# Optimization experiments

Measured on AMD Instinct MI355X. Metric: run time of the kernel, lower is better.

Reference implementation:

```python
import jax, jax.numpy as jnp
import numpy as np

B, A, F, T = 4096, 64, 124, 8
H1, H2 = 64, 16


def setup_inputs() -> dict:
    key = jax.random.key(0)
    ks = jax.random.split(key, 10)
    x = jax.random.normal(ks[0], (B, A, F + 1), dtype=jnp.float32)
    types = jax.random.randint(ks[1], (B, A), 0, T).astype(jnp.float32)
    x = x.at[:, :, 0].set(types)  # column 0 stores atom-type index
    mask = (jax.random.uniform(ks[2], (B, A)) < 0.9).astype(jnp.float32)
    s1 = 1.0 / np.sqrt(F)
    s2 = 1.0 / np.sqrt(H1)
    s3 = 1.0 / np.sqrt(H2)
    return {
        "x_padded": x,
        "mask": mask,
        "W1": jax.random.normal(ks[3], (T, F, H1), dtype=jnp.float32) * s1,
        "b1": jax.random.normal(ks[4], (T, H1), dtype=jnp.float32) * s1,
        "W2": jax.random.normal(ks[5], (T, H1, H2), dtype=jnp.float32) * s2,
        "b2": jax.random.normal(ks[6], (T, H2), dtype=jnp.float32) * s2,
        "W3": jax.random.normal(ks[7], (T, H2, 1), dtype=jnp.float32) * s3,
        "b3": jax.random.normal(ks[8], (T, 1), dtype=jnp.float32) * s3,
    }


def reference(x_padded, mask, W1, b1, W2, b2, W3, b3):
    # x_padded: [B, A, 1+F]; mask: [B, A]
    type_idx = x_padded[:, :, 0].astype(jnp.int32)           # [B, A]
    feats = x_padded[:, :, 1:]                               # [B, A, F]
    n_types = W1.shape[0]
    # Faithful to the original: every type's subnet runs on the FULL batch
    # with non-matching atoms zero-masked (bias paths still contribute).
    type_mask = (type_idx[None, :, :] == jnp.arange(n_types)[:, None, None]).astype(feats.dtype)  # [T,B,A]
    sel = feats[None, :, :, :] * type_mask[..., None]        # [T,B,A,F]
    h = jax.nn.relu(jnp.einsum('tbaf,tfh->tbah', sel, W1) + b1[:, None, None, :])
    h = jax.nn.relu(jnp.einsum('tbah,thg->tbag', h, W2) + b2[:, None, None, :])
    o = jnp.einsum('tbag,tgo->tbao', h, W3) + b3[:, None, None, :]  # [T,B,A,1]
    per_atom = (o[..., 0] * mask[None, :, :]).sum(axis=0)   # [B, A]
    return per_atom.sum(axis=1, keepdims=True)               # [B, 1]
```

## Files before the change

### kernel.cpp

```cpp
#include <hip/hip_runtime.h>
#include <stdint.h>

#define NMOL 4096
#define NATOMS (NMOL * 64)
#define NF 124
#define NT 8
#define ROWV 125
#define CAP 65536

#define WS_DCONST  0
#define WS_CURSOR  64
#define WS_W1S     128
#define WS_W2T     131200
#define WS_LIST    147712

#define HS 72

typedef __attribute__((ext_vector_type(8))) short short8;
typedef __attribute__((ext_vector_type(4))) float floatx4;
typedef __attribute__((ext_vector_type(4), aligned(4))) float floatx4u;
typedef __attribute__((ext_vector_type(4))) unsigned int uint4v;

__device__ __forceinline__ unsigned short f2bf(float f) {
    unsigned u = __builtin_bit_cast(unsigned, f);
    u += 0x7fffu + ((u >> 16) & 1u);
    return (unsigned short)(u >> 16);
}
__device__ __forceinline__ unsigned pk2(float a, float b) {
    return (unsigned)f2bf(a) | ((unsigned)f2bf(b) << 16);
}
__device__ __forceinline__ void ld_lds16(const void* g, void* lds) {
    __builtin_amdgcn_global_load_lds(
        (const __attribute__((address_space(1))) unsigned int*)g,
        (__attribute__((address_space(3))) unsigned int*)lds, 16, 0, 0);
}

__global__ __launch_bounds__(256) void k_setup(const float* __restrict__ W1,
                                               const float* __restrict__ b1,
                                               const float* __restrict__ W2,
                                               const float* __restrict__ b2,
                                               const float* __restrict__ W3,
                                               const float* __restrict__ b3,
                                               float* __restrict__ dconst,
                                               unsigned* __restrict__ cursor,
                                               unsigned short* __restrict__ W1S,
                                               unsigned short* __restrict__ W2T,
                                               float* __restrict__ out) {
    int tid = threadIdx.x, b = blockIdx.x;
    if (b == 0) {
        __shared__ float c[NT];
        if (tid < 128) {
            int t = tid >> 4, g = tid & 15;
            float acc = b2[t * 16 + g];
            for (int h = 0; h < 64; ++h) {
                float h1 = b1[t * 64 + h];
                h1 = h1 > 0.f ? h1 : 0.f;
                acc += h1 * W2[(size_t)t * 1024 + h * 16 + g];
            }
            float h2 = acc > 0.f ? acc : 0.f;
            float v = h2 * W3[t * 16 + g];
            #pragma unroll
            for (int off = 1; off < 16; off <<= 1) v += __shfl_xor(v, off);
            if (g == 0) c[t] = v + b3[t];
        }
        if (tid < NT) cursor[tid] = (unsigned)(tid * CAP);
        __syncthreads();
        if (tid == 0) {
            float T_ = 0.f;
            for (int i = 0; i < NT; ++i) T_ += c[i];
            for (int i = 0; i < NT; ++i) dconst[i] = T_ - c[i] + b3[i];
        }
    } else if (b <= 8) {
        int t = b - 1;
        const float* w1g = W1 + (size_t)t * NF * 64;
        unsigned short* dst = W1S + (size_t)t * 8192;
        for (int id = tid; id < 1024; id += 256) {
            int h = id >> 4, cc = id & 15;
            unsigned u[4];
            #pragma unroll
            for (int j = 0; j < 4; ++j) {
                int f0 = cc * 8 + 2 * j;
                unsigned short lo = (f0 < NF)     ? f2bf(w1g[f0 * 64 + h])       : (unsigned short)0;
                unsigned short hi = (f0 + 1 < NF) ? f2bf(w1g[(f0 + 1) * 64 + h]) : (unsigned short)0;
                u[j] = (unsigned)lo | ((unsigned)hi << 16);
            }
            int p = cc ^ (h & 15);
            *(uint4v*)(dst + h * 128 + p * 8) = (uint4v){u[0], u[1], u[2], u[3]};
        }
        unsigned short* d2 = W2T + (size_t)t * 1024;
        for (int i = tid; i < 1024; i += 256) {
            int g = i >> 6, h = i & 63;
            d2[i] = f2bf(W2[(size_t)t * 1024 + h * 16 + g]);
        }
    } else {
        out[(b - 9) * 256 + tid] = 0.0f;
    }
}

__global__ __launch_bounds__(256) void k_sort(const float* __restrict__ x,
                                              const float* __restrict__ mask,
                                              unsigned* __restrict__ cursor,
                                              unsigned* __restrict__ list) {
    __shared__ unsigned hist[NT], basep[NT], cur[NT];
    int tid = threadIdx.x;
    if (tid < NT) { hist[tid] = 0u; cur[tid] = 0u; }
    __syncthreads();
    int base = blockIdx.x * 1024;
    unsigned char tb[4];
    for (int i = 0; i < 4; ++i) {
        int atom = base + i * 256 + tid;
        float tf = x[(size_t)atom * ROWV];
        float m  = mask[atom];
        tb[i] = 0xFF;
        if (m != 0.0f) { tb[i] = (unsigned char)(int)tf; atomicAdd(&hist[tb[i]], 1u); }
    }
    __syncthreads();
    if (tid < NT && hist[tid]) basep[tid] = atomicAdd(&cursor[tid], hist[tid]);
    __syncthreads();
    for (int i = 0; i < 4; ++i) {
        if (tb[i] != 0xFF) {
            unsigned p = basep[tb[i]] + atomicAdd(&cur[tb[i]], 1u);
            list[p] = (unsigned)(base + i * 256 + tid);
        }
    }
}

__global__ __launch_bounds__(256, 4) void k_mlp(const float* __restrict__ x,
                                                const unsigned short* __restrict__ W1S,
                                                const float* __restrict__ b1,
                                                const unsigned short* __restrict__ W2T,
                                                const float* __restrict__ b2,
                                                const float* __restrict__ W3,
                                                const unsigned* __restrict__ cursor,
                                                const float* __restrict__ dconst,
                                                const unsigned* __restrict__ list,
                                                float* __restrict__ out) {
    __shared__ unsigned short sW[64 * 128];
    __shared__ unsigned short sH[128 * HS];
    __shared__ unsigned sIds[128];

    int t    = blockIdx.x >> 9;
    int tile = blockIdx.x & 511;
    int cnt  = (int)(cursor[t] - (unsigned)(t * CAP));
    int valid = cnt - (tile << 7);
    if (valid <= 0) return;
    if (valid > 128) valid = 128;
    int rowstart = t * CAP + (tile << 7);

    int tid  = threadIdx.x;
    int wv   = tid >> 6;
    int lane = tid & 63;
    int quad = lane >> 4, l15 = lane & 15;
    int rowbase = wv * 32;

    {
        const char* src = (const char*)W1S + (size_t)t * 16384 + wv * 4096 + lane * 16;
        char*       dst = (char*)sW + wv * 4096;
        #pragma unroll
        for (int i = 0; i < 4; ++i) ld_lds16(src + i * 1024, dst + i * 1024);
    }
    if (tid < 128) sIds[tid] = list[rowstart + (tid < valid ? tid : 0)];

    float b1v[4];
    #pragma unroll
    for (int n = 0; n < 4; ++n) b1v[n] = b1[t * 64 + n * 16 + l15];

    __syncthreads();

    short8 afrag[2][4];
    #pragma unroll
    for (int m = 0; m < 2; ++m) {
        unsigned atom = sIds[rowbase + m * 16 + l15];
        const float* rp = x + (size_t)atom * ROWV + 1;
        #pragma unroll
        for (int ks = 0; ks < 4; ++ks) {
            int k0 = ks * 32 + quad * 8;
            floatx4 f0 = (floatx4)(*(const floatx4u*)(rp + k0));
            floatx4 f1 = (floatx4)0.f;
            if (!(ks == 3 && quad == 3))
                f1 = (floatx4)(*(const floatx4u*)(rp + k0 + 4));
            uint4v uu = (uint4v){pk2(f0[0], f0[1]), pk2(f0[2], f0[3]),
                                 pk2(f1[0], f1[1]), pk2(f1[2], f1[3])};
            afrag[m][ks] = __builtin_bit_cast(short8, uu);
        }
    }

    floatx4 c1[2][4];
    #pragma unroll
    for (int m = 0; m < 2; ++m)
        #pragma unroll
        for (int n = 0; n < 4; ++n) c1[m][n] = (floatx4)0.f;

    #pragma unroll
    for (int ks = 0; ks < 4; ++ks) {
        short8 bf[4];
        #pragma unroll
        for (int n = 0; n < 4; ++n)
            bf[n] = *(const short8*)(sW + (n * 16 + l15) * 128 + (((ks * 4 + quad) ^ l15) << 3));
        #pragma unroll
        for (int n = 0; n < 4; ++n) {
            c1[0][n] = __builtin_amdgcn_mfma_f32_16x16x32_bf16(afrag[0][ks], bf[n], c1[0][n], 0, 0, 0);
            c1[1][n] = __builtin_amdgcn_mfma_f32_16x16x32_bf16(afrag[1][ks], bf[n], c1[1][n], 0, 0, 0);
        }
    }

    #pragma unroll
    for (int m = 0; m < 2; ++m)
        #pragma unroll
        for (int n = 0; n < 4; ++n) {
            int col = n * 16 + l15;
            #pragma unroll
            for (int r = 0; r < 4; ++r) {
                float v = c1[m][n][r] + b1v[n];
                v = v > 0.f ? v : 0.f;
                sH[(rowbase + m * 16 + quad * 4 + r) * HS + col] = f2bf(v);
            }
        }

    const unsigned short* w2t = W2T + (size_t)t * 1024;
    floatx4 c2[2];
    c2[0] = (floatx4)0.f; c2[1] = (floatx4)0.f;
    #pragma unroll
    for (int ks = 0; ks < 2; ++ks) {
        int ko = ks * 32 + quad * 8;
        short8 a0 = *(const short8*)(sH + (rowbase + l15) * HS + ko);
        short8 a1 = *(const short8*)(sH + (rowbase + 16 + l15) * HS + ko);
        short8 bw = *(const short8*)(w2t + l15 * 64 + ko);
        c2[0] = __builtin_amdgcn_mfma_f32_16x16x32_bf16(a0, bw, c2[0], 0, 0, 0);
        c2[1] = __builtin_amdgcn_mfma_f32_16x16x32_bf16(a1, bw, c2[1], 0, 0, 0);
    }

    float b2v = b2[t * 16 + l15];
    float w3v = W3[t * 16 + l15];
    float dct = dconst[t];
    #pragma unroll
    for (int m = 0; m < 2; ++m) {
        float h2v[4];
        #pragma unroll
        for (int r = 0; r < 4; ++r) {
            float v = c2[m][r] + b2v;
            v = v > 0.f ? v : 0.f;
            h2v[r] = v * w3v;
        }
        #pragma unroll
        for (int off = 1; off < 16; off <<= 1)
            #pragma unroll
            for (int r = 0; r < 4; ++r) h2v[r] += __shfl_xor(h2v[r], off);
        if (l15 == 0) {
            #pragma unroll
            for (int r = 0; r < 4; ++r) {
                int row = rowbase + m * 16 + quad * 4 + r;
                if (row < valid) {
                    unsigned atom = sIds[row];
                    atomicAdd(&out[atom >> 6], h2v[r] + dct);
                }
            }
        }
    }
}

extern "C" void kernel_launch(void* const* d_in, const int* in_sizes, int n_in,
                              void* d_out, int out_size, void* d_ws, size_t ws_size,
                              hipStream_t stream) {
    const float* x    = (const float*)d_in[0];
    const float* mask = (const float*)d_in[1];
    const float* W1   = (const float*)d_in[2];
    const float* b1   = (const float*)d_in[3];
    const float* W2   = (const float*)d_in[4];
    const float* b2   = (const float*)d_in[5];
    const float* W3   = (const float*)d_in[6];
    const float* b3   = (const float*)d_in[7];
    float* out = (float*)d_out;

    char* ws = (char*)d_ws;
    float*          dconst = (float*)(ws + WS_DCONST);
    unsigned*       cursor = (unsigned*)(ws + WS_CURSOR);
    unsigned short* W1S    = (unsigned short*)(ws + WS_W1S);
    unsigned short* W2T    = (unsigned short*)(ws + WS_W2T);
    unsigned*       list   = (unsigned*)(ws + WS_LIST);

    k_setup<<<25, 256, 0, stream>>>(W1, b1, W2, b2, W3, b3, dconst, cursor, W1S, W2T, out);
    k_sort<<<256, 256, 0, stream>>>(x, mask, cursor, list);
    k_mlp<<<NT * (CAP / 128), 256, 0, stream>>>(x, W1S, b1, W2T, b2, W3,
                                                cursor, dconst, list, out);
}
```

Measured before the change: 217.3 us.

## Load W1 MFMA fragments directly from global, drop LDS staging and block barrier

Pre-packs W1 in setup into a fragment-ordered layout so each lane can read its MFMA B operand straight from global/L2 instead of staging the 16KB weight tile into LDS. Atom ids move from an LDS array into registers and are distributed with wave shuffles, which removes the block-wide barrier. The lower LDS footprint lets the launch bound rise from 4 to 6 blocks per SIMD for more occupancy. The cost is repeated global or cache reads of the weights by every wave, and possible register pressure under the tighter bound.

Result: slower. 234.3 us (+7.9%).

```diff
diff --git a/kernel.cpp b/kernel.cpp
--- a/kernel.cpp
+++ b/kernel.cpp
@@ -10,7 +10,7 @@
 
 #define WS_DCONST  0
 #define WS_CURSOR  64
-#define WS_W1S     128
+#define WS_W1G     128
 #define WS_W2T     131200
 #define WS_LIST    147712
 
@@ -28,11 +28,6 @@
 }
 __device__ __forceinline__ unsigned pk2(float a, float b) {
     return (unsigned)f2bf(a) | ((unsigned)f2bf(b) << 16);
-}
-__device__ __forceinline__ void ld_lds16(const void* g, void* lds) {
-    __builtin_amdgcn_global_load_lds(
-        (const __attribute__((address_space(1))) unsigned int*)g,
-        (__attribute__((address_space(3))) unsigned int*)lds, 16, 0, 0);
 }
 
 __global__ __launch_bounds__(256) void k_setup(const float* __restrict__ W1,
@@ -43,7 +38,7 @@
                                                const float* __restrict__ b3,
                                                float* __restrict__ dconst,
                                                unsigned* __restrict__ cursor,
-                                               unsigned short* __restrict__ W1S,
+                                               unsigned short* __restrict__ W1G,
                                                unsigned short* __restrict__ W2T,
                                                float* __restrict__ out) {
     int tid = threadIdx.x, b = blockIdx.x;
@@ -73,19 +68,20 @@
     } else if (b <= 8) {
         int t = b - 1;
         const float* w1g = W1 + (size_t)t * NF * 64;
-        unsigned short* dst = W1S + (size_t)t * 8192;
+        unsigned short* dst = W1G + (size_t)t * 8192;
         for (int id = tid; id < 1024; id += 256) {
-            int h = id >> 4, cc = id & 15;
+            int l15 = id & 15, n = (id >> 4) & 3, quad = (id >> 6) & 3, ks = id >> 8;
+            int h = n * 16 + l15;
+            int k0 = ks * 32 + quad * 8;
             unsigned u[4];
             #pragma unroll
             for (int j = 0; j < 4; ++j) {
-                int f0 = cc * 8 + 2 * j;
-                unsigned short lo = (f0 < NF)     ? f2bf(w1g[f0 * 64 + h])       : (unsigned short)0;
-                unsigned short hi = (f0 + 1 < NF) ? f2bf(w1g[(f0 + 1) * 64 + h]) : (unsigned short)0;
+                int ka = k0 + 2 * j, kb = k0 + 2 * j + 1;
+                unsigned short lo = (ka < NF) ? f2bf(w1g[ka * 64 + h]) : (unsigned short)0;
+                unsigned short hi = (kb < NF) ? f2bf(w1g[kb * 64 + h]) : (unsigned short)0;
                 u[j] = (unsigned)lo | ((unsigned)hi << 16);
             }
-            int p = cc ^ (h & 15);
-            *(uint4v*)(dst + h * 128 + p * 8) = (uint4v){u[0], u[1], u[2], u[3]};
+            *(uint4v*)(dst + id * 8) = (uint4v){u[0], u[1], u[2], u[3]};
         }
         unsigned short* d2 = W2T + (size_t)t * 1024;
         for (int i = tid; i < 1024; i += 256) {
@@ -125,8 +121,8 @@
     }
 }
 
-__global__ __launch_bounds__(256, 4) void k_mlp(const float* __restrict__ x,
-                                                const unsigned short* __restrict__ W1S,
+__global__ __launch_bounds__(256, 6) void k_mlp(const float* __restrict__ x,
+                                                const unsigned short* __restrict__ W1G,
                                                 const float* __restrict__ b1,
                                                 const unsigned short* __restrict__ W2T,
                                                 const float* __restrict__ b2,
@@ -135,9 +131,7 @@
                                                 const float* __restrict__ dconst,
                                                 const unsigned* __restrict__ list,
                                                 float* __restrict__ out) {
-    __shared__ unsigned short sW[64 * 128];
     __shared__ unsigned short sH[128 * HS];
-    __shared__ unsigned sIds[128];
 
     int t    = blockIdx.x >> 9;
     int tile = blockIdx.x & 511;
@@ -153,24 +147,20 @@
     int quad = lane >> 4, l15 = lane & 15;
     int rowbase = wv * 32;
 
-    {
-        const char* src = (const char*)W1S + (size_t)t * 16384 + wv * 4096 + lane * 16;
-        char*       dst = (char*)sW + wv * 4096;
-        #pragma unroll
-        for (int i = 0; i < 4; ++i) ld_lds16(src + i * 1024, dst + i * 1024);
-    }
-    if (tid < 128) sIds[tid] = list[rowstart + (tid < valid ? tid : 0)];
+    unsigned myid = 0;
+    if (lane < 32) {
+        int row = rowbase + lane;
+        myid = list[rowstart + (row < valid ? row : 0)];
+    }
 
     float b1v[4];
     #pragma unroll
     for (int n = 0; n < 4; ++n) b1v[n] = b1[t * 64 + n * 16 + l15];
 
-    __syncthreads();
-
     short8 afrag[2][4];
     #pragma unroll
     for (int m = 0; m < 2; ++m) {
-        unsigned atom = sIds[rowbase + m * 16 + l15];
+        unsigned atom = (unsigned)__shfl((int)myid, m * 16 + l15);
         const float* rp = x + (size_t)atom * ROWV + 1;
         #pragma unroll
         for (int ks = 0; ks < 4; ++ks) {
@@ -185,6 +175,7 @@
         }
     }
 
+    const unsigned short* w1t = W1G + (size_t)t * 8192;
     floatx4 c1[2][4];
     #pragma unroll
     for (int m = 0; m < 2; ++m)
@@ -196,7 +187,7 @@
         short8 bf[4];
         #pragma unroll
         for (int n = 0; n < 4; ++n)
-            bf[n] = *(const short8*)(sW + (n * 16 + l15) * 128 + (((ks * 4 + quad) ^ l15) << 3));
+            bf[n] = *(const short8*)(w1t + (size_t)(ks * 256 + quad * 64 + n * 16 + l15) * 8);
         #pragma unroll
         for (int n = 0; n < 4; ++n) {
             c1[0][n] = __builtin_amdgcn_mfma_f32_16x16x32_bf16(afrag[0][ks], bf[n], c1[0][n], 0, 0, 0);
@@ -233,6 +224,12 @@
     float b2v = b2[t * 16 + l15];
     float w3v = W3[t * 16 + l15];
     float dct = dconst[t];
+    unsigned ratom[2][4];
+    #pragma unroll
+    for (int m = 0; m < 2; ++m)
+        #pragma unroll
+        for (int r = 0; r < 4; ++r)
+            ratom[m][r] = (unsigned)__shfl((int)myid, m * 16 + quad * 4 + r);
     #pragma unroll
     for (int m = 0; m < 2; ++m) {
         float h2v[4];
@@ -250,10 +247,8 @@
             #pragma unroll
             for (int r = 0; r < 4; ++r) {
                 int row = rowbase + m * 16 + quad * 4 + r;
-                if (row < valid) {
-                    unsigned atom = sIds[row];
-                    atomicAdd(&out[atom >> 6], h2v[r] + dct);
-                }
+                if (row < valid)
+                    atomicAdd(&out[ratom[m][r] >> 6], h2v[r] + dct);
             }
         }
     }
@@ -275,12 +270,12 @@
     char* ws = (char*)d_ws;
     float*          dconst = (float*)(ws + WS_DCONST);
     unsigned*       cursor = (unsigned*)(ws + WS_CURSOR);
-    unsigned short* W1S    = (unsigned short*)(ws + WS_W1S);
+    unsigned short* W1G    = (unsigned short*)(ws + WS_W1G);
     unsigned short* W2T    = (unsigned short*)(ws + WS_W2T);
     unsigned*       list   = (unsigned*)(ws + WS_LIST);
 
-    k_setup<<<25, 256, 0, stream>>>(W1, b1, W2, b2, W3, b3, dconst, cursor, W1S, W2T, out);
+    k_setup<<<25, 256, 0, stream>>>(W1, b1, W2, b2, W3, b3, dconst, cursor, W1G, W2T, out);
     k_sort<<<256, 256, 0, stream>>>(x, mask, cursor, list);
-    k_mlp<<<NT * (CAP / 128), 256, 0, stream>>>(x, W1S, b1, W2T, b2, W3,
+    k_mlp<<<NT * (CAP / 128), 256, 0, stream>>>(x, W1G, b1, W2T, b2, W3,
                                                 cursor, dconst, list, out);
 }
```
